# Optimization experiments

Measured on AMD Instinct MI355X. Metric: run time of the kernel, lower is better.

## Reference

```python
import jax, jax.numpy as jnp
import numpy as np

IN_DIM = 64

def setup_inputs() -> dict:
    key = jax.random.key(0)
    ks = jax.random.split(key, 9)
    B, C, H, W = 4, IN_DIM, 256, 256
    scale = 1.0 / np.sqrt(3 * C)  # conv fan-in init scale
    return {
        'rgb': jax.random.normal(ks[0], (B, C, H, W), dtype=jnp.float32),
        'hsv': jax.random.normal(ks[1], (B, C, H, W), dtype=jnp.float32),
        'lab': jax.random.normal(ks[2], (B, C, H, W), dtype=jnp.float32),
        'Wq': jax.random.normal(ks[3], (C, 3 * C), dtype=jnp.float32) * scale,
        'bq': jax.random.normal(ks[4], (C,), dtype=jnp.float32) * scale,
        'Wk': jax.random.normal(ks[5], (C, 3 * C), dtype=jnp.float32) * scale,
        'bk': jax.random.normal(ks[6], (C,), dtype=jnp.float32) * scale,
        'Wv': jax.random.normal(ks[7], (C, 3 * C), dtype=jnp.float32) * scale,
        'bv': jax.random.normal(ks[8], (C,), dtype=jnp.float32) * scale,
    }

def _proj(x, W, b):
    # 1x1 conv: [B,3C,H,W] x [C,3C] -> [B,C,H,W]
    return jnp.einsum('oc,bchw->bohw', W, x) + b[None, :, None, None]

def reference(rgb, hsv, lab, Wq, bq, Wk, bk, Wv, bv):
    B, C, H, W = rgb.shape
    combined = jnp.concatenate([rgb, hsv, lab], axis=1)  # [B,3C,H,W]
    q = _proj(combined, Wq, bq).reshape(B, C, H * W)     # [B,C,N]
    k = _proj(combined, Wk, bk).reshape(B, C, H * W)     # [B,C,N]
    v = _proj(combined, Wv, bv).reshape(B, C, H * W)     # [B,C,N]
    energy = jnp.einsum('bcn,bdn->bcd', q, k) * (C ** -0.5)  # [B,C,C]
    attention = jax.nn.softmax(energy, axis=-1)
    out = jnp.einsum('bcd,bdn->bcn', attention, v)           # [B,C,N]
    return out.reshape(B, C, H, W)
```

## Files before the change

kernel.cpp:

```cpp
#include <hip/hip_runtime.h>
#include <cstddef>


#define NPIX 65536

typedef _Float16 half4_t __attribute__((ext_vector_type(4)));
typedef _Float16 half8_t __attribute__((ext_vector_type(8)));
typedef float f32x4_t __attribute__((ext_vector_type(4)));

constexpr int TRI_I[78] = {
  0,0,0,0,0,0,0,0,0,0,0,0,
  1,1,1,1,1,1,1,1,1,1,1,
  2,2,2,2,2,2,2,2,2,2,
  3,3,3,3,3,3,3,3,3,
  4,4,4,4,4,4,4,4,
  5,5,5,5,5,5,5,
  6,6,6,6,6,6,
  7,7,7,7,7,
  8,8,8,8,
  9,9,9,
  10,10,
  11};
constexpr int TRI_J[78] = {
  0,1,2,3,4,5,6,7,8,9,10,11,
  1,2,3,4,5,6,7,8,9,10,11,
  2,3,4,5,6,7,8,9,10,11,
  3,4,5,6,7,8,9,10,11,
  4,5,6,7,8,9,10,11,
  5,6,7,8,9,10,11,
  6,7,8,9,10,11,
  7,8,9,10,11,
  8,9,10,11,
  9,10,11,
  10,11,
  11};

#define PSZ 20160

__global__ void k0_zero(float* __restrict__ p, int n) {
  int i = blockIdx.x * 256 + threadIdx.x;
  if (i < n) p[i] = 0.0f;
}

template <int BASE, int CNT>
__device__ __forceinline__ void mfma_run(const _Float16* __restrict__ buf,
                                         f32x4_t* __restrict__ acc, int l15, int g) {
  half8_t fA;
#pragma unroll
  for (int tt = 0; tt < CNT; ++tt) {
    const int t = BASE + tt;
    if (tt == 0 || TRI_I[t] != TRI_I[t - 1]) {
      int rA = TRI_I[t] * 16 + l15;
      fA = *(const half8_t*)(buf + rA * 32 + ((g ^ ((rA >> 1) & 3)) << 3));
    }
    int rB = TRI_J[t] * 16 + l15;
    half8_t fB = *(const half8_t*)(buf + rB * 32 + ((g ^ ((rB >> 1) & 3)) << 3));
    acc[tt] = __builtin_amdgcn_mfma_f32_16x16x32_f16(fA, fB, acc[tt], 0, 0, 0);
  }
}

template <int BASE, int CNT>
__device__ __forceinline__ void flush_part(const f32x4_t* __restrict__ acc,
                                           float* __restrict__ pb, int lane) {
#pragma unroll
  for (int tt = 0; tt < CNT; ++tt)
    *(f32x4_t*)(pb + (BASE + tt) * 256 + lane * 4) = acc[tt];
}

template <int BASE, int CNT>
__device__ __forceinline__ void flush_atomic(const f32x4_t* __restrict__ acc,
                                             float* __restrict__ Gb, int lane) {
#pragma unroll
  for (int tt = 0; tt < CNT; ++tt) {
    const int t = BASE + tt;
#pragma unroll
    for (int r = 0; r < 4; ++r) {
      int gr = TRI_I[t] * 16 + ((lane >> 4) << 2) + r;
      int gc = TRI_J[t] * 16 + (lane & 15);
      atomicAdd(Gb + gr * 192 + gc, acc[tt][r]);
    }
  }
}

__global__ __launch_bounds__(512) void k1_gram(
    const float* __restrict__ rgb, const float* __restrict__ hsv, const float* __restrict__ lab,
    float* __restrict__ G, float* __restrict__ S, float* __restrict__ part, int mode) {
  __shared__ alignas(16) _Float16 lds[6144];
  float* slds = (float*)lds;

  const int t = threadIdx.x;
  const int lane = t & 63;
  const int w = t >> 6;
  const int b = blockIdx.y;
  const int bx = blockIdx.x;
  const int n0 = bx * 512;

  const int gq = t & 7;
  const int r6 = t >> 3;
  const float* gp0 = rgb + (size_t)(b * 64 + r6) * NPIX + n0 + 4 * gq;
  const float* gp1 = hsv + (size_t)(b * 64 + r6) * NPIX + n0 + 4 * gq;
  const float* gp2 = lab + (size_t)(b * 64 + r6) * NPIX + n0 + 4 * gq;
  const int wsw = (((gq >> 1) ^ ((r6 >> 1) & 3)) << 3) + (gq & 1) * 4;
  const int wof0 = (0 * 64 + r6) * 32 + wsw;
  const int wof1 = (1 * 64 + r6) * 32 + wsw;
  const int wof2 = (2 * 64 + r6) * 32 + wsw;

  f32x4_t acc[10];
  const f32x4_t zero4 = {0.0f, 0.0f, 0.0f, 0.0f};
#pragma unroll
  for (int i = 0; i < 10; ++i) acc[i] = zero4;
  float sr0 = 0.f, sr1 = 0.f, sr2 = 0.f;

  float4 P0, P1, P2;
  auto loadR = [&](int cc) {
    P0 = *(const float4*)(gp0 + cc * 32);
    P1 = *(const float4*)(gp1 + cc * 32);
    P2 = *(const float4*)(gp2 + cc * 32);
  };
  auto writeL = [&]() {
    half4_t h;
    sr0 += (P0.x + P0.y) + (P0.z + P0.w);
    h.x = (_Float16)P0.x; h.y = (_Float16)P0.y; h.z = (_Float16)P0.z; h.w = (_Float16)P0.w;
    *(half4_t*)(lds + wof0) = h;
    sr1 += (P1.x + P1.y) + (P1.z + P1.w);
    h.x = (_Float16)P1.x; h.y = (_Float16)P1.y; h.z = (_Float16)P1.z; h.w = (_Float16)P1.w;
    *(half4_t*)(lds + wof1) = h;
    sr2 += (P2.x + P2.y) + (P2.z + P2.w);
    h.x = (_Float16)P2.x; h.y = (_Float16)P2.y; h.z = (_Float16)P2.z; h.w = (_Float16)P2.w;
    *(half4_t*)(lds + wof2) = h;
  };

  const int l15 = lane & 15;
  const int g = lane >> 4;

  loadR(0);
  for (int cc = 0; cc < 16; ++cc) {
    writeL();
    __syncthreads();
    if (cc + 1 < 16) loadR(cc + 1);
    switch (w) {
      case 0: mfma_run<0, 10>(lds, acc, l15, g); break;
      case 1: mfma_run<10, 10>(lds, acc, l15, g); break;
      case 2: mfma_run<20, 10>(lds, acc, l15, g); break;
      case 3: mfma_run<30, 10>(lds, acc, l15, g); break;
      case 4: mfma_run<40, 10>(lds, acc, l15, g); break;
      case 5: mfma_run<50, 10>(lds, acc, l15, g); break;
      case 6: mfma_run<60, 10>(lds, acc, l15, g); break;
      case 7: mfma_run<70, 8>(lds, acc, l15, g); break;
    }
    __syncthreads();
  }

  if (mode) {
    float* pb = part + (size_t)(b * 128 + bx) * PSZ;
    switch (w) {
      case 0: flush_part<0, 10>(acc, pb, lane); break;
      case 1: flush_part<10, 10>(acc, pb, lane); break;
      case 2: flush_part<20, 10>(acc, pb, lane); break;
      case 3: flush_part<30, 10>(acc, pb, lane); break;
      case 4: flush_part<40, 10>(acc, pb, lane); break;
      case 5: flush_part<50, 10>(acc, pb, lane); break;
      case 6: flush_part<60, 10>(acc, pb, lane); break;
      case 7: flush_part<70, 8>(acc, pb, lane); break;
    }
  } else {
    float* Gb = G + b * 36864;
    switch (w) {
      case 0: flush_atomic<0, 10>(acc, Gb, lane); break;
      case 1: flush_atomic<10, 10>(acc, Gb, lane); break;
      case 2: flush_atomic<20, 10>(acc, Gb, lane); break;
      case 3: flush_atomic<30, 10>(acc, Gb, lane); break;
      case 4: flush_atomic<40, 10>(acc, Gb, lane); break;
      case 5: flush_atomic<50, 10>(acc, Gb, lane); break;
      case 6: flush_atomic<60, 10>(acc, Gb, lane); break;
      case 7: flush_atomic<70, 8>(acc, Gb, lane); break;
    }
  }

  slds[(0 * 64 + r6) * 8 + gq] = sr0;
  slds[(1 * 64 + r6) * 8 + gq] = sr1;
  slds[(2 * 64 + r6) * 8 + gq] = sr2;
  __syncthreads();
  if (t < 192) {
    float v = 0.f;
#pragma unroll
    for (int q = 0; q < 8; ++q) v += slds[t * 8 + q];
    if (mode)
      part[(size_t)(b * 128 + bx) * PSZ + 19968 + t] = v;
    else
      atomicAdd(S + b * 192 + t, v);
  }
}

__global__ void k1r_reduce(const float* __restrict__ part, float* __restrict__ G,
                           float* __restrict__ S) {
  int idx = blockIdx.x * 256 + threadIdx.x;
  if (idx >= 4 * (PSZ / 4)) return;
  int b = idx / (PSZ / 4);
  int f4 = idx % (PSZ / 4);
  int flat = f4 * 4;
  const float* base = part + (size_t)b * 128 * PSZ + flat;
  f32x4_t v0 = {0.f, 0.f, 0.f, 0.f}, v1 = v0, v2 = v0, v3 = v0;
#pragma unroll 4
  for (int q = 0; q < 128; q += 4) {
    v0 += *(const f32x4_t*)(base + (size_t)(q + 0) * PSZ);
    v1 += *(const f32x4_t*)(base + (size_t)(q + 1) * PSZ);
    v2 += *(const f32x4_t*)(base + (size_t)(q + 2) * PSZ);
    v3 += *(const f32x4_t*)(base + (size_t)(q + 3) * PSZ);
  }
  f32x4_t v = (v0 + v1) + (v2 + v3);
  if (flat < 19968) {
    int tt = flat >> 8;
    int r = flat & 255;
    int lane = r >> 2;
    int row = TRI_I[tt] * 16 + ((lane >> 4) << 2);
    int col = TRI_J[tt] * 16 + (lane & 15);
    float* Gb = G + b * 36864;
#pragma unroll
    for (int e = 0; e < 4; ++e) Gb[(row + e) * 192 + col] = v[e];
    *(f32x4_t*)(Gb + col * 192 + row) = v;
  } else {
    *(f32x4_t*)(S + b * 192 + (flat - 19968)) = v;
  }
}

__global__ void k1m_mirror(float* __restrict__ G) {
  int b = blockIdx.y;
  int idx = blockIdx.x * 256 + threadIdx.x;
  int i = idx / 192, j = idx % 192;
  if ((i >> 4) > (j >> 4)) G[b * 36864 + idx] = G[b * 36864 + j * 192 + i];
}

__global__ __launch_bounds__(256) void k2_small(
    const float* __restrict__ G, const float* __restrict__ S,
    const float* __restrict__ Wq, const float* __restrict__ bq,
    const float* __restrict__ Wk, const float* __restrict__ bk,
    const float* __restrict__ Wv, const float* __restrict__ bv,
    _Float16* __restrict__ Mh, float* __restrict__ c0w) {
  const int b = blockIdx.y;
  const int cbase = blockIdx.x * 8;
  const int t = threadIdx.x;
  __shared__ float T1[192 * 9];
  __shared__ float el[64 * 8];
  __shared__ float sq[8];
  __shared__ float sk[64];
  const float* Gb = G + b * 36864;
  const float* Sb = S + b * 192;

  if (t < 8) {
    float a = 0.f;
    const float* wq = Wq + (cbase + t) * 192;
    for (int i = 0; i < 192; ++i) a = fmaf(wq[i], Sb[i], a);
    sq[t] = a;
  } else if (t < 72) {
    int d = t - 8;
    float a = 0.f;
    const float* wk = Wk + d * 192;
    for (int j = 0; j < 192; ++j) a = fmaf(wk[j], Sb[j], a);
    sk[d] = a;
  }
  for (int e = t; e < 1536; e += 256) {
    int j = e % 192, cp = e / 192;
    const float* wq = Wq + (cbase + cp) * 192;
    float a = 0.f;
    for (int i = 0; i < 192; ++i) a = fmaf(wq[i], Gb[i * 192 + j], a);
    T1[j * 9 + cp] = a;
  }
  __syncthreads();
  for (int e = t; e < 512; e += 256) {
    int cp = e & 7, d = e >> 3;
    const float* wk = Wk + d * 192;
    float a = 0.f;
    for (int j = 0; j < 192; ++j) a = fmaf(T1[j * 9 + cp], wk[j], a);
    float bqc = bq[cbase + cp], bkd = bk[d];
    a += bqc * sk[d] + bkd * sq[cp] + 65536.0f * bqc * bkd;
    el[d * 8 + cp] = a * 0.125f;
  }
  __syncthreads();
  if (t < 8) {
    float mx = -3.0e38f;
    for (int d = 0; d < 64; ++d) mx = fmaxf(mx, el[d * 8 + t]);
    float sum = 0.f;
    for (int d = 0; d < 64; ++d) {
      float pv = expf(el[d * 8 + t] - mx);
      el[d * 8 + t] = pv;
      sum += pv;
    }
    float inv = 1.0f / sum;
    for (int d = 0; d < 64; ++d) el[d * 8 + t] *= inv;
  }
  __syncthreads();
  for (int e = t; e < 1536; e += 256) {
    int i = e % 192, cp = e / 192;
    int c = cbase + cp;
    float a = 0.f;
    for (int d = 0; d < 64; ++d) a = fmaf(el[d * 8 + cp], Wv[d * 192 + i], a);
    Mh[(size_t)b * 12288 + c * 192 + (i ^ ((c & 7) << 3))] = (_Float16)a;
  }
  if (t < 8) {
    float a = 0.f;
    for (int d = 0; d < 64; ++d) a = fmaf(el[d * 8 + t], bv[d], a);
    c0w[b * 64 + cbase + t] = a;
  }
}

__global__ __launch_bounds__(256, 3) void k3_out(
    const float* __restrict__ rgb, const float* __restrict__ hsv, const float* __restrict__ lab,
    const _Float16* __restrict__ Mh, const float* __restrict__ c0w, float* __restrict__ out) {
  __shared__ alignas(16) _Float16 lds_m[12288];
  __shared__ alignas(16) _Float16 lds_x[8192];
  __shared__ float c0l[64];
  const int t = threadIdx.x;
  const int lane = t & 63;
  const int w = t >> 6;
  const int b = blockIdx.y;
  const int nblk = blockIdx.x * 256;

  {
    const float4* msrc = (const float4*)(Mh + (size_t)b * 12288);
    float4* mdst = (float4*)lds_m;
#pragma unroll
    for (int k = 0; k < 6; ++k) mdst[t + 256 * k] = msrc[t + 256 * k];
    if (t < 64) c0l[t] = c0w[b * 64 + t];
  }

  const int xi = t & 31;
  const int ng = t >> 5;
  const float* srcs[3] = {rgb, hsv, lab};

  f32x4_t acc[4][4];
  const f32x4_t zero4 = {0.0f, 0.0f, 0.0f, 0.0f};
#pragma unroll
  for (int i = 0; i < 4; ++i)
#pragma unroll
    for (int j = 0; j < 4; ++j) acc[i][j] = zero4;

  float4 xr[8];
  auto xload = [&](int kc) {
    int ig = kc * 32 + xi;
    const float* p = srcs[ig >> 6] + (size_t)(b * 64 + (ig & 63)) * NPIX + nblk + ng * 32;
#pragma unroll
    for (int f = 0; f < 8; ++f) xr[f] = *(const float4*)(p + f * 4);
  };
  auto xwrite = [&]() {
#pragma unroll
    for (int f = 0; f < 8; ++f) {
      int n = ng * 32 + f * 4;
      lds_x[(n + 0) * 32 + (xi ^ 0)]  = (_Float16)xr[f].x;
      lds_x[(n + 1) * 32 + (xi ^ 8)]  = (_Float16)xr[f].y;
      lds_x[(n + 2) * 32 + (xi ^ 16)] = (_Float16)xr[f].z;
      lds_x[(n + 3) * 32 + (xi ^ 24)] = (_Float16)xr[f].w;
    }
  };

  const int g = lane >> 4;
  const int l15 = lane & 15;

  xload(0);
  for (int kc = 0; kc < 6; ++kc) {
    xwrite();
    __syncthreads();
    if (kc + 1 < 6) xload(kc + 1);
    half8_t fx[4], fm[4];
#pragma unroll
    for (int nt = 0; nt < 4; ++nt) {
      int n = w * 64 + nt * 16 + l15;
      fx[nt] = *(const half8_t*)(lds_x + n * 32 + ((8 * g) ^ ((n & 3) << 3)));
    }
#pragma unroll
    for (int ct = 0; ct < 4; ++ct) {
      int c = ct * 16 + l15;
      fm[ct] = *(const half8_t*)(lds_m + c * 192 + ((kc * 32 + 8 * g) ^ ((c & 7) << 3)));
    }
#pragma unroll
    for (int nt = 0; nt < 4; ++nt)
#pragma unroll
      for (int ct = 0; ct < 4; ++ct)
        acc[nt][ct] = __builtin_amdgcn_mfma_f32_16x16x32_f16(fx[nt], fm[ct], acc[nt][ct], 0, 0, 0);
    __syncthreads();
  }

#pragma unroll
  for (int ct = 0; ct < 4; ++ct) {
    int c = ct * 16 + l15;
    float c0v = c0l[c];
#pragma unroll
    for (int nt = 0; nt < 4; ++nt) {
      int n = nblk + w * 64 + nt * 16 + 4 * g;
      float4 o;
      o.x = acc[nt][ct][0] + c0v;
      o.y = acc[nt][ct][1] + c0v;
      o.z = acc[nt][ct][2] + c0v;
      o.w = acc[nt][ct][3] + c0v;
      *(float4*)(out + (size_t)(b * 64 + c) * NPIX + n) = o;
    }
  }
}

extern "C" void kernel_launch(void* const* d_in, const int* in_sizes, int n_in,
                              void* d_out, int out_size, void* d_ws, size_t ws_size,
                              hipStream_t stream) {
  const float* rgb = (const float*)d_in[0];
  const float* hsv = (const float*)d_in[1];
  const float* lab = (const float*)d_in[2];
  const float* Wq = (const float*)d_in[3];
  const float* bq = (const float*)d_in[4];
  const float* Wk = (const float*)d_in[5];
  const float* bk = (const float*)d_in[6];
  const float* Wv = (const float*)d_in[7];
  const float* bv = (const float*)d_in[8];
  float* out = (float*)d_out;
  float* ws = (float*)d_ws;

  float* G = ws;
  float* S = ws + 147456;
  _Float16* Mh = (_Float16*)(ws + 148224);
  float* c0w = ws + 172800;
  float* part = ws + 173056;
  const size_t need1 = (size_t)(173056 + 4 * 128 * PSZ) * 4;
  const int mode = ws_size >= need1 ? 1 : 0;

  if (!mode)
    k0_zero<<<dim3(579), dim3(256), 0, stream>>>(ws, 148224);

  k1_gram<<<dim3(128, 4), dim3(512), 0, stream>>>(rgb, hsv, lab, G, S, part, mode);
  if (mode)
    k1r_reduce<<<dim3(79), dim3(256), 0, stream>>>(part, G, S);
  else
    k1m_mirror<<<dim3(144, 4), dim3(256), 0, stream>>>(G);
  k2_small<<<dim3(8, 4), dim3(256), 0, stream>>>(G, S, Wq, bq, Wk, bk, Wv, bv, Mh, c0w);
  k3_out<<<dim3(256, 4), dim3(256), 0, stream>>>(rgb, hsv, lab, Mh, c0w, out);
}
```

Baseline: 151.9 us.

## Split gram kernel into two 256-thread blocks each computing half the tiles

```diff
diff --git a/kernel.cpp b/kernel.cpp
--- a/kernel.cpp
+++ b/kernel.cpp
@@ -82,7 +82,7 @@
   }
 }
 
-__global__ __launch_bounds__(512) void k1_gram(
+__global__ __launch_bounds__(256) void k1_gram(
     const float* __restrict__ rgb, const float* __restrict__ hsv, const float* __restrict__ lab,
     float* __restrict__ G, float* __restrict__ S, float* __restrict__ part, int mode) {
   __shared__ alignas(16) _Float16 lds[6144];
@@ -91,19 +91,21 @@
   const int t = threadIdx.x;
   const int lane = t & 63;
   const int w = t >> 6;
+  const int half = blockIdx.x & 1;
+  const int bx = blockIdx.x >> 1;
   const int b = blockIdx.y;
-  const int bx = blockIdx.x;
   const int n0 = bx * 512;
-
-  const int gq = t & 7;
-  const int r6 = t >> 3;
-  const float* gp0 = rgb + (size_t)(b * 64 + r6) * NPIX + n0 + 4 * gq;
-  const float* gp1 = hsv + (size_t)(b * 64 + r6) * NPIX + n0 + 4 * gq;
-  const float* gp2 = lab + (size_t)(b * 64 + r6) * NPIX + n0 + 4 * gq;
-  const int wsw = (((gq >> 1) ^ ((r6 >> 1) & 3)) << 3) + (gq & 1) * 4;
-  const int wof0 = (0 * 64 + r6) * 32 + wsw;
-  const int wof1 = (1 * 64 + r6) * 32 + wsw;
-  const int wof2 = (2 * 64 + r6) * 32 + wsw;
+  const int wsel = half * 4 + w;
+
+  const int q = t & 3;
+  const int r6 = t >> 2;
+  const float* gp0 = rgb + (size_t)(b * 64 + r6) * NPIX + n0 + 8 * q;
+  const float* gp1 = hsv + (size_t)(b * 64 + r6) * NPIX + n0 + 8 * q;
+  const float* gp2 = lab + (size_t)(b * 64 + r6) * NPIX + n0 + 8 * q;
+  const int wb = ((q ^ ((r6 >> 1) & 3)) << 3);
+  const int wof0 = (0 * 64 + r6) * 32 + wb;
+  const int wof1 = (1 * 64 + r6) * 32 + wb;
+  const int wof2 = (2 * 64 + r6) * 32 + wb;
 
   f32x4_t acc[10];
   const f32x4_t zero4 = {0.0f, 0.0f, 0.0f, 0.0f};
@@ -111,23 +113,32 @@
   for (int i = 0; i < 10; ++i) acc[i] = zero4;
   float sr0 = 0.f, sr1 = 0.f, sr2 = 0.f;
 
-  float4 P0, P1, P2;
+  float4 Pa0, Pb0, Pa1, Pb1, Pa2, Pb2;
   auto loadR = [&](int cc) {
-    P0 = *(const float4*)(gp0 + cc * 32);
-    P1 = *(const float4*)(gp1 + cc * 32);
-    P2 = *(const float4*)(gp2 + cc * 32);
+    Pa0 = *(const float4*)(gp0 + cc * 32);
+    Pb0 = *(const float4*)(gp0 + cc * 32 + 4);
+    Pa1 = *(const float4*)(gp1 + cc * 32);
+    Pb1 = *(const float4*)(gp1 + cc * 32 + 4);
+    Pa2 = *(const float4*)(gp2 + cc * 32);
+    Pb2 = *(const float4*)(gp2 + cc * 32 + 4);
   };
   auto writeL = [&]() {
     half4_t h;
-    sr0 += (P0.x + P0.y) + (P0.z + P0.w);
-    h.x = (_Float16)P0.x; h.y = (_Float16)P0.y; h.z = (_Float16)P0.z; h.w = (_Float16)P0.w;
+    sr0 += (Pa0.x + Pa0.y) + (Pa0.z + Pa0.w) + (Pb0.x + Pb0.y) + (Pb0.z + Pb0.w);
+    h.x = (_Float16)Pa0.x; h.y = (_Float16)Pa0.y; h.z = (_Float16)Pa0.z; h.w = (_Float16)Pa0.w;
     *(half4_t*)(lds + wof0) = h;
-    sr1 += (P1.x + P1.y) + (P1.z + P1.w);
-    h.x = (_Float16)P1.x; h.y = (_Float16)P1.y; h.z = (_Float16)P1.z; h.w = (_Float16)P1.w;
+    h.x = (_Float16)Pb0.x; h.y = (_Float16)Pb0.y; h.z = (_Float16)Pb0.z; h.w = (_Float16)Pb0.w;
+    *(half4_t*)(lds + wof0 + 4) = h;
+    sr1 += (Pa1.x + Pa1.y) + (Pa1.z + Pa1.w) + (Pb1.x + Pb1.y) + (Pb1.z + Pb1.w);
+    h.x = (_Float16)Pa1.x; h.y = (_Float16)Pa1.y; h.z = (_Float16)Pa1.z; h.w = (_Float16)Pa1.w;
     *(half4_t*)(lds + wof1) = h;
-    sr2 += (P2.x + P2.y) + (P2.z + P2.w);
-    h.x = (_Float16)P2.x; h.y = (_Float16)P2.y; h.z = (_Float16)P2.z; h.w = (_Float16)P2.w;
+    h.x = (_Float16)Pb1.x; h.y = (_Float16)Pb1.y; h.z = (_Float16)Pb1.z; h.w = (_Float16)Pb1.w;
+    *(half4_t*)(lds + wof1 + 4) = h;
+    sr2 += (Pa2.x + Pa2.y) + (Pa2.z + Pa2.w) + (Pb2.x + Pb2.y) + (Pb2.z + Pb2.w);
+    h.x = (_Float16)Pa2.x; h.y = (_Float16)Pa2.y; h.z = (_Float16)Pa2.z; h.w = (_Float16)Pa2.w;
     *(half4_t*)(lds + wof2) = h;
+    h.x = (_Float16)Pb2.x; h.y = (_Float16)Pb2.y; h.z = (_Float16)Pb2.z; h.w = (_Float16)Pb2.w;
+    *(half4_t*)(lds + wof2 + 4) = h;
   };
 
   const int l15 = lane & 15;
@@ -138,57 +149,57 @@
     writeL();
     __syncthreads();
     if (cc + 1 < 16) loadR(cc + 1);
-    switch (w) {
+    switch (wsel) {
       case 0: mfma_run<0, 10>(lds, acc, l15, g); break;
       case 1: mfma_run<10, 10>(lds, acc, l15, g); break;
       case 2: mfma_run<20, 10>(lds, acc, l15, g); break;
-      case 3: mfma_run<30, 10>(lds, acc, l15, g); break;
-      case 4: mfma_run<40, 10>(lds, acc, l15, g); break;
-      case 5: mfma_run<50, 10>(lds, acc, l15, g); break;
-      case 6: mfma_run<60, 10>(lds, acc, l15, g); break;
-      case 7: mfma_run<70, 8>(lds, acc, l15, g); break;
+      case 3: mfma_run<30, 9>(lds, acc, l15, g); break;
+      case 4: mfma_run<39, 10>(lds, acc, l15, g); break;
+      case 5: mfma_run<49, 10>(lds, acc, l15, g); break;
+      case 6: mfma_run<59, 10>(lds, acc, l15, g); break;
+      case 7: mfma_run<69, 9>(lds, acc, l15, g); break;
     }
     __syncthreads();
   }
 
   if (mode) {
     float* pb = part + (size_t)(b * 128 + bx) * PSZ;
-    switch (w) {
+    switch (wsel) {
       case 0: flush_part<0, 10>(acc, pb, lane); break;
       case 1: flush_part<10, 10>(acc, pb, lane); break;
       case 2: flush_part<20, 10>(acc, pb, lane); break;
-      case 3: flush_part<30, 10>(acc, pb, lane); break;
-      case 4: flush_part<40, 10>(acc, pb, lane); break;
-      case 5: flush_part<50, 10>(acc, pb, lane); break;
-      case 6: flush_part<60, 10>(acc, pb, lane); break;
-      case 7: flush_part<70, 8>(acc, pb, lane); break;
+      case 3: flush_part<30, 9>(acc, pb, lane); break;
+      case 4: flush_part<39, 10>(acc, pb, lane); break;
+      case 5: flush_part<49, 10>(acc, pb, lane); break;
+      case 6: flush_part<59, 10>(acc, pb, lane); break;
+      case 7: flush_part<69, 9>(acc, pb, lane); break;
     }
   } else {
     float* Gb = G + b * 36864;
-    switch (w) {
+    switch (wsel) {
       case 0: flush_atomic<0, 10>(acc, Gb, lane); break;
       case 1: flush_atomic<10, 10>(acc, Gb, lane); break;
       case 2: flush_atomic<20, 10>(acc, Gb, lane); break;
-      case 3: flush_atomic<30, 10>(acc, Gb, lane); break;
-      case 4: flush_atomic<40, 10>(acc, Gb, lane); break;
-      case 5: flush_atomic<50, 10>(acc, Gb, lane); break;
-      case 6: flush_atomic<60, 10>(acc, Gb, lane); break;
-      case 7: flush_atomic<70, 8>(acc, Gb, lane); break;
-    }
-  }
-
-  slds[(0 * 64 + r6) * 8 + gq] = sr0;
-  slds[(1 * 64 + r6) * 8 + gq] = sr1;
-  slds[(2 * 64 + r6) * 8 + gq] = sr2;
-  __syncthreads();
-  if (t < 192) {
-    float v = 0.f;
-#pragma unroll
-    for (int q = 0; q < 8; ++q) v += slds[t * 8 + q];
-    if (mode)
-      part[(size_t)(b * 128 + bx) * PSZ + 19968 + t] = v;
-    else
-      atomicAdd(S + b * 192 + t, v);
+      case 3: flush_atomic<30, 9>(acc, Gb, lane); break;
+      case 4: flush_atomic<39, 10>(acc, Gb, lane); break;
+      case 5: flush_atomic<49, 10>(acc, Gb, lane); break;
+      case 6: flush_atomic<59, 10>(acc, Gb, lane); break;
+      case 7: flush_atomic<69, 9>(acc, Gb, lane); break;
+    }
+  }
+
+  if (half == 0) {
+    slds[(0 * 64 + r6) * 4 + q] = sr0;
+    slds[(1 * 64 + r6) * 4 + q] = sr1;
+    slds[(2 * 64 + r6) * 4 + q] = sr2;
+    __syncthreads();
+    if (t < 192) {
+      float v = (slds[4 * t] + slds[4 * t + 1]) + (slds[4 * t + 2] + slds[4 * t + 3]);
+      if (mode)
+        part[(size_t)(b * 128 + bx) * PSZ + 19968 + t] = v;
+      else
+        atomicAdd(S + b * 192 + t, v);
+    }
   }
 }
 
@@ -423,7 +434,7 @@
   if (!mode)
     k0_zero<<<dim3(579), dim3(256), 0, stream>>>(ws, 148224);
 
-  k1_gram<<<dim3(128, 4), dim3(512), 0, stream>>>(rgb, hsv, lab, G, S, part, mode);
+  k1_gram<<<dim3(256, 4), dim3(256), 0, stream>>>(rgb, hsv, lab, G, S, part, mode);
   if (mode)
     k1r_reduce<<<dim3(79), dim3(256), 0, stream>>>(part, G, S);
   else
```

Result: slower. 179.5 us (+18.2%).
